# Kernel tuning notes

Measured on AMD Instinct MI355X. Metric: run time of the kernel, lower is better.

Reference implementation:

```python
import jax, jax.numpy as jnp
import numpy as np

B, N, D, S, H = 32, 4096, 256, 16, 512
ITERS = 3
EPS = 1e-8
LN_EPS = 1e-5  # torch LayerNorm default


def _ln(x, w, b):
    m = jnp.mean(x, axis=-1, keepdims=True)
    v = jnp.mean(jnp.square(x - m), axis=-1, keepdims=True)
    return (x - m) / jnp.sqrt(v + LN_EPS) * w + b


def setup_inputs() -> dict:
    key = jax.random.key(0)
    ks = jax.random.split(key, 20)
    s = 1.0 / np.sqrt(D)
    return {
        "inputs": jax.random.normal(ks[0], (B, N, D), jnp.float32),
        "token_weight": jax.random.uniform(ks[1], (B, N), jnp.float32),
        "noise": jax.random.normal(ks[2], (B, S, D), jnp.float32),
        "ln_in_w": jnp.ones((D,), jnp.float32), "ln_in_b": jnp.zeros((D,), jnp.float32),
        "ln_s_w": jnp.ones((D,), jnp.float32), "ln_s_b": jnp.zeros((D,), jnp.float32),
        "ln_m_w": jnp.ones((D,), jnp.float32), "ln_m_b": jnp.zeros((D,), jnp.float32),
        "Wk": jax.random.normal(ks[3], (D, D), jnp.float32) * s,
        "Wv": jax.random.normal(ks[4], (D, D), jnp.float32) * s,
        "Wq": jax.random.normal(ks[5], (D, D), jnp.float32) * s,
        "gru_wih": jax.random.normal(ks[6], (3 * D, D), jnp.float32) * s,
        "gru_whh": jax.random.normal(ks[7], (3 * D, D), jnp.float32) * s,
        "gru_bih": jax.random.normal(ks[8], (3 * D,), jnp.float32) * s,
        "gru_bhh": jax.random.normal(ks[9], (3 * D,), jnp.float32) * s,
        "mlp_w1": jax.random.normal(ks[10], (H, D), jnp.float32) * s,
        "mlp_b1": jnp.zeros((H,), jnp.float32),
        "mlp_w2": jax.random.normal(ks[11], (D, H), jnp.float32) * (1.0 / np.sqrt(H)),
        "mlp_b2": jnp.zeros((D,), jnp.float32),
        "slots_mu": jax.random.normal(ks[12], (1, 1, D), jnp.float32) * 0.02,
        "slots_logsigma": jax.random.normal(ks[13], (1, 1, D), jnp.float32) * 0.02,
    }


def _gru(x, h, wih, whh, bih, bhh):
    # torch GRUCell: gates ordered r, z, n
    gi = x @ wih.T + bih  # [BS, 3D]
    gh = h @ whh.T + bhh
    ir, iz, inn = jnp.split(gi, 3, axis=-1)
    hr, hz, hn = jnp.split(gh, 3, axis=-1)
    r = jax.nn.sigmoid(ir + hr)
    z = jax.nn.sigmoid(iz + hz)
    n = jnp.tanh(inn + r * hn)
    return (1.0 - z) * n + z * h


def reference(inputs, token_weight, noise, ln_in_w, ln_in_b, ln_s_w, ln_s_b,
              ln_m_w, ln_m_b, Wk, Wv, Wq, gru_wih, gru_whh, gru_bih, gru_bhh,
              mlp_w1, mlp_b1, mlp_w2, mlp_b2, slots_mu, slots_logsigma):
    tw = jnp.clip(token_weight, 0.0, None)  # [B,N]
    x = _ln(inputs, ln_in_w, ln_in_b)
    k = x @ Wk.T  # [B,N,D]
    v = x @ Wv.T
    sigma = jnp.clip(jnp.exp(slots_logsigma), 1e-6, None)
    slots = slots_mu + sigma * noise  # [B,S,D]
    scale = D ** (-0.5)
    attn = None
    for _ in range(ITERS):
        slots_prev = slots
        q = _ln(slots, ln_s_w, ln_s_b) @ Wq.T  # [B,S,D]
        logits = jnp.einsum('bnd,bmd->bnm', k, q) * scale  # [B,N,S]
        attn = jax.nn.softmax(logits, axis=-1)  # softmax over slots
        attn = attn * tw[:, :, None]
        attn = attn / (jnp.sum(attn, axis=1, keepdims=True) + EPS)  # normalize over tokens
        updates = jnp.einsum('bnm,bnd->bmd', attn, v)  # [B,S,D]
        slots = _gru(updates.reshape(B * S, D), slots_prev.reshape(B * S, D),
                     gru_wih, gru_whh, gru_bih, gru_bhh).reshape(B, S, D)
        h = jax.nn.gelu(_ln(slots, ln_m_w, ln_m_b) @ mlp_w1.T + mlp_b1, approximate=False)
        slots = slots + h @ mlp_w2.T + mlp_b2
    return slots, attn
```

## Files before the change

### kernel.cpp

```cpp
#include <hip/hip_runtime.h>
#include <hip/hip_bf16.h>
#include <math.h>


#define EPS_ 1e-8f
#define LNEPS_ 1e-5f
#define XSW(r) ((((r)&7)<<3) ^ ((((r)>>3)&3)<<4))

typedef __attribute__((ext_vector_type(8))) short bf16x8;
typedef __attribute__((ext_vector_type(4))) float f32x4;
typedef __attribute__((ext_vector_type(4))) short s16x4;

static __device__ __forceinline__ short f2bf(float f) {
  __hip_bfloat16 h = __float2bfloat16(f);
  union { __hip_bfloat16 h; short s; } u; u.h = h; return u.s;
}
static __device__ __forceinline__ float4 ld4(const float* p){ return *(const float4*)p; }

__global__ __launch_bounds__(256) void k_prep(
    const float* __restrict__ Wq, const float* __restrict__ Wk,
    const float* __restrict__ wih, const float* __restrict__ Wv,
    const float* __restrict__ whh, const float* __restrict__ w1, const float* __restrict__ w2,
    short* __restrict__ MTb, short* __restrict__ Mb, short* __restrict__ whhb,
    short* __restrict__ w1b, short* __restrict__ w2b) {
  int blk = blockIdx.x, t = threadIdx.x;
  if (blk < 64) {
    int e0 = blk*4;
    float a0=0,a1=0,a2=0,a3=0;
    for (int d=0; d<256; d++) {
      float qv = Wq[d*256 + t];
      a0 += qv*Wk[d*256+e0];   a1 += qv*Wk[d*256+e0+1];
      a2 += qv*Wk[d*256+e0+2]; a3 += qv*Wk[d*256+e0+3];
    }
    MTb[(e0  )*256+t]=f2bf(a0); MTb[(e0+1)*256+t]=f2bf(a1);
    MTb[(e0+2)*256+t]=f2bf(a2); MTb[(e0+3)*256+t]=f2bf(a3);
  } else if (blk < 256) {
    int n0 = (blk-64)*4;
    float a0=0,a1=0,a2=0,a3=0;
    for (int d=0; d<256; d++) {
      float vv = Wv[d*256 + t];
      a0 += wih[(n0  )*256+d]*vv; a1 += wih[(n0+1)*256+d]*vv;
      a2 += wih[(n0+2)*256+d]*vv; a3 += wih[(n0+3)*256+d]*vv;
    }
    Mb[(size_t)(n0  )*256+t]=f2bf(a0); Mb[(size_t)(n0+1)*256+t]=f2bf(a1);
    Mb[(size_t)(n0+2)*256+t]=f2bf(a2); Mb[(size_t)(n0+3)*256+t]=f2bf(a3);
  } else {
    int c = (blk-256)*256 + t;
    const float* src; short* dst;
    if (c < 49152) { src=whh; dst=whhb; }
    else if ((c-=49152) < 32768) { src=w1; dst=w1b; }
    else { c-=32768; src=w2; dst=w2b; }
    float4 v = ld4(src + (size_t)c*4);
    short4 o; o.x=f2bf(v.x); o.y=f2bf(v.y); o.z=f2bf(v.z); o.w=f2bf(v.w);
    *(short4*)(dst + (size_t)c*4) = o;
  }
}

template<int LNIN, int WATTN>
__global__ __launch_bounds__(256) void k3(
    const float* __restrict__ inputs, const float* __restrict__ lnw, const float* __restrict__ lnb,
    short* __restrict__ xbf, const short* __restrict__ qk, const float* __restrict__ twg,
    float* __restrict__ ux_part, float* __restrict__ colsum_part, float* __restrict__ attn_un) {
  __shared__ __align__(16) short Xs[64*256];
  __shared__ __align__(16) short Pt[16*72];
  __shared__ float tws[64];
  __shared__ float cs[16];
  __shared__ float lnwb[512];
  const int t = threadIdx.x;
  const int b = blockIdx.x >> 6;
  const size_t rowbase = (size_t)b*4096 + (blockIdx.x & 63)*64;
  const int lane = t & 63, w = t >> 6, l15 = lane & 15, lg = lane >> 4;
  if (t<64) tws[t] = fmaxf(twg[rowbase + t], 0.f);
  if (t<16) cs[t]=0.f;
  bf16x8 qkf[8];
  {
    const short* qrow = qk + ((size_t)(b*16+l15))*256 + lg*8;
    #pragma unroll
    for (int kk=0;kk<8;kk++) qkf[kk] = *(const bf16x8*)(qrow + kk*32);
  }
  if (LNIN) {
    if (t < 64)       *(float4*)&lnwb[t*4]           = ld4(lnw + t*4);
    else if (t < 128) *(float4*)&lnwb[256+(t-64)*4]  = ld4(lnb + (t-64)*4);
    __syncthreads();
    const float* ing = inputs + rowbase*256;
    const int r = t>>2, c = t&3;
    float4 vv[16];
    #pragma unroll
    for (int k=0;k<16;k++) vv[k] = ld4(ing + r*256 + (c+4*k)*4);
    float s=0.f, sq=0.f;
    #pragma unroll
    for (int k=0;k<16;k++){
      s  += vv[k].x+vv[k].y+vv[k].z+vv[k].w;
      sq += vv[k].x*vv[k].x+vv[k].y*vv[k].y+vv[k].z*vv[k].z+vv[k].w*vv[k].w;
    }
    s += __shfl_xor(s,1);  s += __shfl_xor(s,2);
    sq += __shfl_xor(sq,1); sq += __shfl_xor(sq,2);
    float mean = s*(1.f/256.f);
    float rstd = rsqrtf(sq*(1.f/256.f) - mean*mean + LNEPS_);
    short* xw = xbf + rowbase*256;
    const int sw = XSW(r);
    #pragma unroll
    for (int k=0;k<16;k++){
      int d0 = (c+4*k)*4;
      float4 wv = *(float4*)&lnwb[d0];
      float4 bv = *(float4*)&lnwb[256+d0];
      s16x4 pk;
      pk[0]=f2bf((vv[k].x-mean)*rstd*wv.x+bv.x);
      pk[1]=f2bf((vv[k].y-mean)*rstd*wv.y+bv.y);
      pk[2]=f2bf((vv[k].z-mean)*rstd*wv.z+bv.z);
      pk[3]=f2bf((vv[k].w-mean)*rstd*wv.w+bv.w);
      *(s16x4*)&Xs[r*256 + (d0 ^ sw)] = pk;
      *(s16x4*)&xw[r*256 + d0] = pk;
    }
  } else {
    const int srow = t>>5, sck = t&31;
    uint4 pf[8];
    const short* xg = xbf + rowbase*256;
    #pragma unroll
    for (int r8=0;r8<8;r8++)
      pf[r8] = *(const uint4*)&xg[(size_t)(r8*8+srow)*256 + sck*8];
    #pragma unroll
    for (int r8=0;r8<8;r8++){
      int row = r8*8+srow;
      *(uint4*)&Xs[row*256 + ((sck*8) ^ XSW(row))] = pf[r8];
    }
  }
  __syncthreads();
  f32x4 acc = {0.f,0.f,0.f,0.f};
  {
    const int ra = w*16+l15, sa = XSW(ra);
    #pragma unroll
    for (int kk=0;kk<8;kk++){
      bf16x8 af = *(const bf16x8*)&Xs[ra*256 + ((kk*32+lg*8) ^ sa)];
      acc = __builtin_amdgcn_mfma_f32_16x16x32_bf16(af, qkf[kk], acc, 0,0,0);
    }
  }
  float a4[4];
  #pragma unroll
  for (int q=0;q<4;q++){
    float v = acc[q]*0.0625f;
    float m = v;
    #pragma unroll
    for (int d=1; d<16; d<<=1) m = fmaxf(m, __shfl_xor(m, d, 16));
    float e = __expf(v-m);
    float se = e;
    #pragma unroll
    for (int d=1; d<16; d<<=1) se += __shfl_xor(se, d, 16);
    int row = w*16 + lg*4 + q;
    float a = (e/se)*tws[row];
    a4[q] = a;
    if (WATTN)
      attn_un[(rowbase + row)*16 + l15] = a;
  }
  float psum = a4[0]+a4[1]+a4[2]+a4[3];
  psum += __shfl_xor(psum, 16);
  psum += __shfl_xor(psum, 32);
  if (lane<16) atomicAdd(&cs[l15], psum);
  s16x4 pk; pk[0]=f2bf(a4[0]); pk[1]=f2bf(a4[1]); pk[2]=f2bf(a4[2]); pk[3]=f2bf(a4[3]);
  *(s16x4*)&Pt[l15*72 + w*16 + lg*4] = pk;
  __syncthreads();
  f32x4 uacc[4] = {};
  #pragma unroll
  for (int kk=0;kk<2;kk++){
    bf16x8 a2 = *(const bf16x8*)&Pt[l15*72 + kk*32 + lg*8];
    #pragma unroll
    for (int tt=0;tt<4;tt++){
      int col = w*64 + tt*16 + l15;
      bf16x8 b2;
      #pragma unroll
      for (int j=0;j<8;j++){
        int r2 = kk*32 + lg*8 + j;
        b2[j] = Xs[r2*256 + (col ^ XSW(r2))];
      }
      uacc[tt] = __builtin_amdgcn_mfma_f32_16x16x32_bf16(a2, b2, uacc[tt], 0,0,0);
    }
  }
  if (t<16) colsum_part[blockIdx.x*16 + t] = cs[t];
  #pragma unroll
  for (int tt=0;tt<4;tt++){
    #pragma unroll
    for (int q=0;q<4;q++)
      ux_part[(size_t)blockIdx.x*4096 + (lg*4+q)*256 + w*64 + tt*16 + l15] = uacc[tt][q];
  }
}

__global__ __launch_bounds__(256) void k_reduce(const float* __restrict__ uxp,
    const float* __restrict__ csp, short* __restrict__ uxr, float* __restrict__ csr) {
  int r = blockIdx.x;
  int b = r>>4, s = r&15;
  int t = threadIdx.x;
  float cs = 0.f;
  #pragma unroll 8
  for (int k=0;k<64;k++) cs += csp[((b<<6)+k)*16 + s];
  float u = 0.f;
  #pragma unroll 8
  for (int k=0;k<64;k++) u += uxp[(size_t)((b<<6)+k)*4096 + s*256 + t];
  uxr[(size_t)r*256+t] = f2bf(u/(cs+EPS_));
  if (t==0) csr[r] = cs;
}

__global__ __launch_bounds__(256) void k_gigh(
    const short* __restrict__ uxr, const short* __restrict__ slotsb,
    const short* __restrict__ Mb, const short* __restrict__ whhb,
    const float* __restrict__ bih, const float* __restrict__ bhh,
    float* __restrict__ gig) {
  __shared__ short As[64*40];
  __shared__ short Ws[64*40];
  const int t=threadIdx.x, bn=blockIdx.x, bm=blockIdx.y;
  const short* A; const short* W; const float* bias; int wo;
  if (bn<12) { A=uxr;    W=Mb   + (size_t)bn*64*256;      bias=bih; wo=bn*64; }
  else       { A=slotsb; W=whhb + (size_t)(bn-12)*64*256; bias=bhh; wo=(bn-12)*64; }
  const int w=t>>6, lane=t&63, l15=lane&15, lg=lane>>4;
  f32x4 acc[4]={};
  for (int k0=0;k0<256;k0+=32){
    __syncthreads();
    *(uint4*)&As[(t>>2)*40+(t&3)*8] = *(const uint4*)&A[(size_t)(bm*64+(t>>2))*256 + k0 + (t&3)*8];
    *(uint4*)&Ws[(t>>2)*40+(t&3)*8] = *(const uint4*)&W[(size_t)(t>>2)*256 + k0 + (t&3)*8];
    __syncthreads();
    bf16x8 af = *(const bf16x8*)&As[(w*16+l15)*40+lg*8];
    #pragma unroll
    for (int ct=0;ct<4;ct++){
      bf16x8 bfr = *(const bf16x8*)&Ws[(ct*16+l15)*40+lg*8];
      acc[ct]=__builtin_amdgcn_mfma_f32_16x16x32_bf16(af,bfr,acc[ct],0,0,0);
    }
  }
  #pragma unroll
  for (int ct=0;ct<4;ct++){
    float bv = bias[wo + ct*16 + l15];
    #pragma unroll
    for (int q=0;q<4;q++){
      int row = bm*64 + w*16 + lg*4 + q;
      gig[(size_t)row*1536 + bn*64 + ct*16 + l15] = acc[ct][q] + bv;
    }
  }
}

__global__ __launch_bounds__(256) void k_mlp1(
    const short* __restrict__ lnmb, const short* __restrict__ w1b,
    const float* __restrict__ b1, short* __restrict__ hb) {
  __shared__ short As[64*40];
  __shared__ short Ws[64*40];
  const int t=threadIdx.x, bn=blockIdx.x, bm=blockIdx.y;
  const int w=t>>6, lane=t&63, l15=lane&15, lg=lane>>4;
  f32x4 acc[4]={};
  for (int k0=0;k0<256;k0+=32){
    __syncthreads();
    *(uint4*)&As[(t>>2)*40+(t&3)*8] = *(const uint4*)&lnmb[(size_t)(bm*64+(t>>2))*256 + k0 + (t&3)*8];
    *(uint4*)&Ws[(t>>2)*40+(t&3)*8] = *(const uint4*)&w1b[(size_t)(bn*64+(t>>2))*256 + k0 + (t&3)*8];
    __syncthreads();
    bf16x8 af = *(const bf16x8*)&As[(w*16+l15)*40+lg*8];
    #pragma unroll
    for (int ct=0;ct<4;ct++){
      bf16x8 bfr = *(const bf16x8*)&Ws[(ct*16+l15)*40+lg*8];
      acc[ct]=__builtin_amdgcn_mfma_f32_16x16x32_bf16(af,bfr,acc[ct],0,0,0);
    }
  }
  #pragma unroll
  for (int ct=0;ct<4;ct++){
    float bv = b1[bn*64 + ct*16 + l15];
    #pragma unroll
    for (int q=0;q<4;q++){
      int row = bm*64 + w*16 + lg*4 + q;
      float v = acc[ct][q] + bv;
      v = 0.5f*v*(1.f+erff(v*0.70710678118654752f));
      hb[(size_t)row*512 + bn*64 + ct*16 + l15] = f2bf(v);
    }
  }
}

__global__ __launch_bounds__(256) void k_gates(const float* __restrict__ gig,
    const float* __restrict__ lw, const float* __restrict__ lb,
    float* __restrict__ slots, short* __restrict__ lnmb) {
  int row  = blockIdx.x*4 + (threadIdx.x>>6);
  int lane = threadIdx.x & 63;
  const float* gi = gig + (size_t)row*1536 + lane*4;
  float4 ir = ld4(gi), iz = ld4(gi+256), inn = ld4(gi+512);
  float4 hr = ld4(gi+768), hz = ld4(gi+1024), hn = ld4(gi+1280);
  float* sp = slots + (size_t)row*256 + lane*4;
  float4 h = ld4(sp);
  float hp[4];
  {
    float r0 = 1.f/(1.f+__expf(-(ir.x+hr.x))); float z0 = 1.f/(1.f+__expf(-(iz.x+hz.x)));
    hp[0] = (1.f-z0)*tanhf(inn.x + r0*hn.x) + z0*h.x;
    float r1 = 1.f/(1.f+__expf(-(ir.y+hr.y))); float z1 = 1.f/(1.f+__expf(-(iz.y+hz.y)));
    hp[1] = (1.f-z1)*tanhf(inn.y + r1*hn.y) + z1*h.y;
    float r2 = 1.f/(1.f+__expf(-(ir.z+hr.z))); float z2 = 1.f/(1.f+__expf(-(iz.z+hz.z)));
    hp[2] = (1.f-z2)*tanhf(inn.z + r2*hn.z) + z2*h.z;
    float r3 = 1.f/(1.f+__expf(-(ir.w+hr.w))); float z3 = 1.f/(1.f+__expf(-(iz.w+hz.w)));
    hp[3] = (1.f-z3)*tanhf(inn.w + r3*hn.w) + z3*h.w;
  }
  float s = hp[0]+hp[1]+hp[2]+hp[3];
  float sq = hp[0]*hp[0]+hp[1]*hp[1]+hp[2]*hp[2]+hp[3]*hp[3];
  #pragma unroll
  for (int d=1; d<64; d<<=1) { s += __shfl_xor(s,d); sq += __shfl_xor(sq,d); }
  float mean = s*(1.f/256.f);
  float rstd = rsqrtf(sq*(1.f/256.f) - mean*mean + LNEPS_);
  float4 wv = ld4(lw+lane*4), bv = ld4(lb+lane*4);
  *(float4*)sp = make_float4(hp[0],hp[1],hp[2],hp[3]);
  short4 o;
  o.x = f2bf((hp[0]-mean)*rstd*wv.x+bv.x);
  o.y = f2bf((hp[1]-mean)*rstd*wv.y+bv.y);
  o.z = f2bf((hp[2]-mean)*rstd*wv.z+bv.z);
  o.w = f2bf((hp[3]-mean)*rstd*wv.w+bv.w);
  *(short4*)(lnmb + (size_t)row*256 + lane*4) = o;
}

template<int MODE>
__global__ __launch_bounds__(256) void k_slotend(
    const short* __restrict__ hb, const short* __restrict__ w2b, const float* __restrict__ b2,
    const float* __restrict__ mu, const float* __restrict__ ls, const float* __restrict__ noise,
    const float* __restrict__ res, float* __restrict__ sout, short* __restrict__ slotsb,
    const float* __restrict__ lnsw, const float* __restrict__ lnsb,
    const short* __restrict__ MTb, short* __restrict__ qk) {
  __shared__ short As[64*40];
  __shared__ short Ws[256*40];
  __shared__ short lnS[64*264];
  const int t=threadIdx.x, bm=blockIdx.x;
  const int w=t>>6, lane=t&63, l15=lane&15, lg=lane>>4;
  float v[16][4];
  if (MODE==1) {
    #pragma unroll
    for (int ct=0;ct<16;ct++){
      int col = ct*16+l15;
      float m = mu[col], sg = fmaxf(__expf(ls[col]),1e-6f);
      #pragma unroll
      for (int q=0;q<4;q++){
        int row = bm*64 + w*16 + lg*4 + q;
        v[ct][q] = m + sg*noise[(size_t)row*256+col];
      }
    }
  } else {
    f32x4 acc[16]={};
    for (int k0=0;k0<512;k0+=32){
      __syncthreads();
      *(uint4*)&As[(t>>2)*40+(t&3)*8] = *(const uint4*)&hb[(size_t)(bm*64+(t>>2))*512 + k0 + (t&3)*8];
      #pragma unroll
      for (int i=0;i<4;i++){ int idx=t+i*256;
        *(uint4*)&Ws[(idx>>2)*40+(idx&3)*8] = *(const uint4*)&w2b[(size_t)(idx>>2)*512 + k0 + (idx&3)*8]; }
      __syncthreads();
      bf16x8 af = *(const bf16x8*)&As[(w*16+l15)*40+lg*8];
      #pragma unroll
      for (int ct=0;ct<16;ct++){
        bf16x8 bfr = *(const bf16x8*)&Ws[(ct*16+l15)*40+lg*8];
        acc[ct]=__builtin_amdgcn_mfma_f32_16x16x32_bf16(af,bfr,acc[ct],0,0,0);
      }
    }
    #pragma unroll
    for (int ct=0;ct<16;ct++){
      int col = ct*16+l15;
      float bv = b2[col];
      #pragma unroll
      for (int q=0;q<4;q++){
        int row = bm*64 + w*16 + lg*4 + q;
        v[ct][q] = acc[ct][q] + bv + res[(size_t)row*256+col];
      }
    }
  }
  float s[4]={0,0,0,0}, sq[4]={0,0,0,0};
  #pragma unroll
  for (int ct=0;ct<16;ct++)
    #pragma unroll
    for (int q=0;q<4;q++){ s[q]+=v[ct][q]; sq[q]+=v[ct][q]*v[ct][q]; }
  #pragma unroll
  for (int q=0;q<4;q++){
    #pragma unroll
    for (int d=1; d<16; d<<=1){ s[q]+=__shfl_xor(s[q],d,16); sq[q]+=__shfl_xor(sq[q],d,16); }
  }
  #pragma unroll
  for (int ct=0;ct<16;ct++){
    int col = ct*16+l15;
    float lw = (MODE!=2) ? lnsw[col] : 0.f;
    float lb = (MODE!=2) ? lnsb[col] : 0.f;
    #pragma unroll
    for (int q=0;q<4;q++){
      int row = bm*64 + w*16 + lg*4 + q;
      sout[(size_t)row*256+col] = v[ct][q];
      if (MODE!=2){
        float mean = s[q]*(1.f/256.f);
        float rstd = rsqrtf(sq[q]*(1.f/256.f)-mean*mean+LNEPS_);
        slotsb[(size_t)row*256+col] = f2bf(v[ct][q]);
        lnS[(w*16+lg*4+q)*264 + col] = f2bf((v[ct][q]-mean)*rstd*lw+lb);
      }
    }
  }
  if (MODE!=2){
    f32x4 qa[16]={};
    for (int k0=0;k0<256;k0+=32){
      __syncthreads();
      #pragma unroll
      for (int i=0;i<4;i++){ int idx=t+i*256;
        *(uint4*)&Ws[(idx>>2)*40+(idx&3)*8] = *(const uint4*)&MTb[(size_t)(idx>>2)*256 + k0 + (idx&3)*8]; }
      __syncthreads();
      bf16x8 af = *(const bf16x8*)&lnS[(w*16+l15)*264 + k0 + lg*8];
      #pragma unroll
      for (int ct=0;ct<16;ct++){
        bf16x8 bfr = *(const bf16x8*)&Ws[(ct*16+l15)*40+lg*8];
        qa[ct]=__builtin_amdgcn_mfma_f32_16x16x32_bf16(af,bfr,qa[ct],0,0,0);
      }
    }
    #pragma unroll
    for (int ct=0;ct<16;ct++)
      #pragma unroll
      for (int q=0;q<4;q++)
        qk[(size_t)(bm*64+w*16+lg*4+q)*256 + ct*16+l15] = f2bf(qa[ct][q]);
  }
}

__global__ __launch_bounds__(256) void k_attn_norm(float* __restrict__ au,
    const float* __restrict__ cs) {
  size_t i = ((size_t)blockIdx.x*256 + threadIdx.x)*4;
  float4 v = ld4(au + i);
  int s = (int)(i & 15);
  size_t b = i >> 16;
  const float* c = cs + b*16 + s;
  float4 o;
  o.x = v.x/(c[0]+EPS_); o.y = v.y/(c[1]+EPS_);
  o.z = v.z/(c[2]+EPS_); o.w = v.w/(c[3]+EPS_);
  *(float4*)(au + i) = o;
}

extern "C" void kernel_launch(void* const* d_in, const int* in_sizes, int n_in,
                              void* d_out, int out_size, void* d_ws, size_t ws_size,
                              hipStream_t stream) {
  const float* inputs   = (const float*)d_in[0];
  const float* token_w  = (const float*)d_in[1];
  const float* noise    = (const float*)d_in[2];
  const float* ln_in_w  = (const float*)d_in[3];
  const float* ln_in_b  = (const float*)d_in[4];
  const float* ln_s_w   = (const float*)d_in[5];
  const float* ln_s_b   = (const float*)d_in[6];
  const float* ln_m_w   = (const float*)d_in[7];
  const float* ln_m_b   = (const float*)d_in[8];
  const float* Wk       = (const float*)d_in[9];
  const float* Wv       = (const float*)d_in[10];
  const float* Wq       = (const float*)d_in[11];
  const float* gru_wih  = (const float*)d_in[12];
  const float* gru_whh  = (const float*)d_in[13];
  const float* gru_bih  = (const float*)d_in[14];
  const float* gru_bhh  = (const float*)d_in[15];
  const float* mlp_w1   = (const float*)d_in[16];
  const float* mlp_b1   = (const float*)d_in[17];
  const float* mlp_w2   = (const float*)d_in[18];
  const float* mlp_b2   = (const float*)d_in[19];
  const float* slots_mu = (const float*)d_in[20];
  const float* slots_ls = (const float*)d_in[21];

  float* out_slots = (float*)d_out;
  float* out_attn  = out_slots + 131072;

  char* wsb = (char*)d_ws;
  size_t off = 0;
  short* xbf     = (short*)(wsb + off); off += 67108864;
  float* ux_part = (float*)(wsb + off); off += 33554432;
  float* cs_part = (float*)(wsb + off); off += 131072;
  float* cs_red  = (float*)(wsb + off); off += 2048;
  short* qk      = (short*)(wsb + off); off += 262144;
  short* uxr     = (short*)(wsb + off); off += 262144;
  short* MTb     = (short*)(wsb + off); off += 131072;
  short* Mb      = (short*)(wsb + off); off += 393216;
  float* gig     = (float*)(wsb + off); off += 3145728;
  float* slots   = (float*)(wsb + off); off += 524288;
  short* slotsb  = (short*)(wsb + off); off += 262144;
  short* lnmb    = (short*)(wsb + off); off += 262144;
  short* hb      = (short*)(wsb + off); off += 524288;
  short* whhb    = (short*)(wsb + off); off += 393216;
  short* w1b     = (short*)(wsb + off); off += 262144;
  short* w2b     = (short*)(wsb + off); off += 262144;

  k_prep<<<704,256,0,stream>>>(Wq, Wk, gru_wih, Wv, gru_whh, mlp_w1, mlp_w2,
                               MTb, Mb, whhb, w1b, w2b);
  k_slotend<1><<<8,256,0,stream>>>(nullptr, nullptr, nullptr, slots_mu, slots_ls, noise,
                                   nullptr, slots, slotsb, ln_s_w, ln_s_b, MTb, qk);
  for (int it=0; it<3; ++it) {
    if (it==0)
      k3<1,0><<<2048,256,0,stream>>>(inputs, ln_in_w, ln_in_b, xbf, qk, token_w,
                                     ux_part, cs_part, out_attn);
    else if (it==1)
      k3<0,0><<<2048,256,0,stream>>>(inputs, ln_in_w, ln_in_b, xbf, qk, token_w,
                                     ux_part, cs_part, out_attn);
    else
      k3<0,1><<<2048,256,0,stream>>>(inputs, ln_in_w, ln_in_b, xbf, qk, token_w,
                                     ux_part, cs_part, out_attn);
    k_reduce<<<512,256,0,stream>>>(ux_part, cs_part, uxr, cs_red);
    k_gigh<<<dim3(24,8),256,0,stream>>>(uxr, slotsb, Mb, whhb, gru_bih, gru_bhh, gig);
    k_gates<<<128,256,0,stream>>>(gig, ln_m_w, ln_m_b, slots, lnmb);
    k_mlp1<<<dim3(8,8),256,0,stream>>>(lnmb, w1b, mlp_b1, hb);
    if (it<2)
      k_slotend<0><<<8,256,0,stream>>>(hb, w2b, mlp_b2, nullptr, nullptr, nullptr,
                                       slots, slots, slotsb, ln_s_w, ln_s_b, MTb, qk);
    else
      k_slotend<2><<<8,256,0,stream>>>(hb, w2b, mlp_b2, nullptr, nullptr, nullptr,
                                       slots, out_slots, slotsb, ln_s_w, ln_s_b, MTb, qk);
  }
  k_attn_norm<<<2048,256,0,stream>>>(out_attn, cs_red);
}
```

Measured before the change: 262.0 us.

## Halve k3 row tile to 32 and store partial updates as bf16

The k3 attention kernel now processes 32 tokens per block instead of 64 and launches twice as many blocks with a launch-bounds occupancy hint. LDS use drops, but only two of four waves do the logits/softmax MFMA. Per-block partial update sums are staged through shared memory and written as bf16 with vector stores, and k_reduce sums 128 bf16 partials per batch instead of 64 fp32 ones. The aim is higher occupancy and less partial-sum traffic, at the cost of more partials to reduce, idle waves in the first phase, and lower precision in the accumulated partials.

```diff
diff --git a/kernel.cpp b/kernel.cpp
--- a/kernel.cpp
+++ b/kernel.cpp
@@ -14,6 +14,9 @@
 static __device__ __forceinline__ short f2bf(float f) {
   __hip_bfloat16 h = __float2bfloat16(f);
   union { __hip_bfloat16 h; short s; } u; u.h = h; return u.s;
+}
+static __device__ __forceinline__ float bf2f(short s) {
+  union { float f; unsigned u; } x; x.u = ((unsigned)(unsigned short)s) << 16; return x.f;
 }
 static __device__ __forceinline__ float4 ld4(const float* p){ return *(const float4*)p; }
 
@@ -57,23 +60,23 @@
 }
 
 template<int LNIN, int WATTN>
-__global__ __launch_bounds__(256) void k3(
+__global__ __launch_bounds__(256, 6) void k3(
     const float* __restrict__ inputs, const float* __restrict__ lnw, const float* __restrict__ lnb,
     short* __restrict__ xbf, const short* __restrict__ qk, const float* __restrict__ twg,
-    float* __restrict__ ux_part, float* __restrict__ colsum_part, float* __restrict__ attn_un) {
-  __shared__ __align__(16) short Xs[64*256];
-  __shared__ __align__(16) short Pt[16*72];
-  __shared__ float tws[64];
+    short* __restrict__ ux_part, float* __restrict__ colsum_part, float* __restrict__ attn_un) {
+  __shared__ __align__(16) short Xs[32*256];
+  __shared__ __align__(16) short Pt[16*40];
+  __shared__ float tws[32];
   __shared__ float cs[16];
   __shared__ float lnwb[512];
   const int t = threadIdx.x;
-  const int b = blockIdx.x >> 6;
-  const size_t rowbase = (size_t)b*4096 + (blockIdx.x & 63)*64;
+  const int b = blockIdx.x >> 7;
+  const size_t rowbase = (size_t)b*4096 + (blockIdx.x & 127)*32;
   const int lane = t & 63, w = t >> 6, l15 = lane & 15, lg = lane >> 4;
-  if (t<64) tws[t] = fmaxf(twg[rowbase + t], 0.f);
+  if (t<32) tws[t] = fmaxf(twg[rowbase + t], 0.f);
   if (t<16) cs[t]=0.f;
   bf16x8 qkf[8];
-  {
+  if (w<2) {
     const short* qrow = qk + ((size_t)(b*16+l15))*256 + lg*8;
     #pragma unroll
     for (int kk=0;kk<8;kk++) qkf[kk] = *(const bf16x8*)(qrow + kk*32);
@@ -83,25 +86,25 @@
     else if (t < 128) *(float4*)&lnwb[256+(t-64)*4]  = ld4(lnb + (t-64)*4);
     __syncthreads();
     const float* ing = inputs + rowbase*256;
-    const int r = t>>2, c = t&3;
-    float4 vv[16];
-    #pragma unroll
-    for (int k=0;k<16;k++) vv[k] = ld4(ing + r*256 + (c+4*k)*4);
+    const int r = t>>3, c = t&7;
+    float4 vv[8];
+    #pragma unroll
+    for (int k=0;k<8;k++) vv[k] = ld4(ing + r*256 + (c+8*k)*4);
     float s=0.f, sq=0.f;
     #pragma unroll
-    for (int k=0;k<16;k++){
+    for (int k=0;k<8;k++){
       s  += vv[k].x+vv[k].y+vv[k].z+vv[k].w;
       sq += vv[k].x*vv[k].x+vv[k].y*vv[k].y+vv[k].z*vv[k].z+vv[k].w*vv[k].w;
     }
-    s += __shfl_xor(s,1);  s += __shfl_xor(s,2);
-    sq += __shfl_xor(sq,1); sq += __shfl_xor(sq,2);
+    s += __shfl_xor(s,1);  s += __shfl_xor(s,2);  s += __shfl_xor(s,4);
+    sq += __shfl_xor(sq,1); sq += __shfl_xor(sq,2); sq += __shfl_xor(sq,4);
     float mean = s*(1.f/256.f);
     float rstd = rsqrtf(sq*(1.f/256.f) - mean*mean + LNEPS_);
     short* xw = xbf + rowbase*256;
     const int sw = XSW(r);
     #pragma unroll
-    for (int k=0;k<16;k++){
-      int d0 = (c+4*k)*4;
+    for (int k=0;k<8;k++){
+      int d0 = (c+8*k)*4;
       float4 wv = *(float4*)&lnwb[d0];
       float4 bv = *(float4*)&lnwb[256+d0];
       s16x4 pk;
@@ -113,88 +116,95 @@
       *(s16x4*)&xw[r*256 + d0] = pk;
     }
   } else {
-    const int srow = t>>5, sck = t&31;
-    uint4 pf[8];
+    uint4 pf[4];
     const short* xg = xbf + rowbase*256;
     #pragma unroll
-    for (int r8=0;r8<8;r8++)
-      pf[r8] = *(const uint4*)&xg[(size_t)(r8*8+srow)*256 + sck*8];
-    #pragma unroll
-    for (int r8=0;r8<8;r8++){
-      int row = r8*8+srow;
-      *(uint4*)&Xs[row*256 + ((sck*8) ^ XSW(row))] = pf[r8];
+    for (int i=0;i<4;i++){
+      int idx = t + i*256;
+      pf[i] = *(const uint4*)&xg[(size_t)(idx>>5)*256 + (idx&31)*8];
+    }
+    #pragma unroll
+    for (int i=0;i<4;i++){
+      int idx = t + i*256, row = idx>>5;
+      *(uint4*)&Xs[row*256 + (((idx&31)*8) ^ XSW(row))] = pf[i];
     }
   }
   __syncthreads();
-  f32x4 acc = {0.f,0.f,0.f,0.f};
-  {
+  if (w<2) {
+    f32x4 acc = {0.f,0.f,0.f,0.f};
     const int ra = w*16+l15, sa = XSW(ra);
     #pragma unroll
     for (int kk=0;kk<8;kk++){
       bf16x8 af = *(const bf16x8*)&Xs[ra*256 + ((kk*32+lg*8) ^ sa)];
       acc = __builtin_amdgcn_mfma_f32_16x16x32_bf16(af, qkf[kk], acc, 0,0,0);
     }
-  }
-  float a4[4];
-  #pragma unroll
-  for (int q=0;q<4;q++){
-    float v = acc[q]*0.0625f;
-    float m = v;
-    #pragma unroll
-    for (int d=1; d<16; d<<=1) m = fmaxf(m, __shfl_xor(m, d, 16));
-    float e = __expf(v-m);
-    float se = e;
-    #pragma unroll
-    for (int d=1; d<16; d<<=1) se += __shfl_xor(se, d, 16);
-    int row = w*16 + lg*4 + q;
-    float a = (e/se)*tws[row];
-    a4[q] = a;
-    if (WATTN)
-      attn_un[(rowbase + row)*16 + l15] = a;
-  }
-  float psum = a4[0]+a4[1]+a4[2]+a4[3];
-  psum += __shfl_xor(psum, 16);
-  psum += __shfl_xor(psum, 32);
-  if (lane<16) atomicAdd(&cs[l15], psum);
-  s16x4 pk; pk[0]=f2bf(a4[0]); pk[1]=f2bf(a4[1]); pk[2]=f2bf(a4[2]); pk[3]=f2bf(a4[3]);
-  *(s16x4*)&Pt[l15*72 + w*16 + lg*4] = pk;
+    float a4[4];
+    #pragma unroll
+    for (int q=0;q<4;q++){
+      float v = acc[q]*0.0625f;
+      float m = v;
+      #pragma unroll
+      for (int d=1; d<16; d<<=1) m = fmaxf(m, __shfl_xor(m, d, 16));
+      float e = __expf(v-m);
+      float se = e;
+      #pragma unroll
+      for (int d=1; d<16; d<<=1) se += __shfl_xor(se, d, 16);
+      int row = w*16 + lg*4 + q;
+      float a = (e/se)*tws[row];
+      a4[q] = a;
+      if (WATTN)
+        attn_un[(rowbase + row)*16 + l15] = a;
+    }
+    float psum = a4[0]+a4[1]+a4[2]+a4[3];
+    psum += __shfl_xor(psum, 16);
+    psum += __shfl_xor(psum, 32);
+    if (lane<16) atomicAdd(&cs[l15], psum);
+    s16x4 pk; pk[0]=f2bf(a4[0]); pk[1]=f2bf(a4[1]); pk[2]=f2bf(a4[2]); pk[3]=f2bf(a4[3]);
+    *(s16x4*)&Pt[l15*40 + w*16 + lg*4] = pk;
+  }
   __syncthreads();
   f32x4 uacc[4] = {};
-  #pragma unroll
-  for (int kk=0;kk<2;kk++){
-    bf16x8 a2 = *(const bf16x8*)&Pt[l15*72 + kk*32 + lg*8];
+  {
+    bf16x8 a2 = *(const bf16x8*)&Pt[l15*40 + lg*8];
     #pragma unroll
     for (int tt=0;tt<4;tt++){
       int col = w*64 + tt*16 + l15;
       bf16x8 b2;
       #pragma unroll
       for (int j=0;j<8;j++){
-        int r2 = kk*32 + lg*8 + j;
+        int r2 = lg*8 + j;
         b2[j] = Xs[r2*256 + (col ^ XSW(r2))];
       }
       uacc[tt] = __builtin_amdgcn_mfma_f32_16x16x32_bf16(a2, b2, uacc[tt], 0,0,0);
     }
   }
   if (t<16) colsum_part[blockIdx.x*16 + t] = cs[t];
-  #pragma unroll
-  for (int tt=0;tt<4;tt++){
+  __syncthreads();
+  #pragma unroll
+  for (int tt=0;tt<4;tt++)
     #pragma unroll
     for (int q=0;q<4;q++)
-      ux_part[(size_t)blockIdx.x*4096 + (lg*4+q)*256 + w*64 + tt*16 + l15] = uacc[tt][q];
-  }
-}
-
-__global__ __launch_bounds__(256) void k_reduce(const float* __restrict__ uxp,
+      Xs[(lg*4+q)*256 + w*64 + tt*16 + l15] = f2bf(uacc[tt][q]);
+  __syncthreads();
+  short* up = ux_part + (size_t)blockIdx.x*4096;
+  #pragma unroll
+  for (int i=0;i<2;i++){
+    int idx = t + i*256;
+    *(uint4*)&up[idx*8] = *(const uint4*)&Xs[idx*8];
+  }
+}
+
+__global__ __launch_bounds__(256) void k_reduce(const short* __restrict__ uxp,
     const float* __restrict__ csp, short* __restrict__ uxr, float* __restrict__ csr) {
   int r = blockIdx.x;
   int b = r>>4, s = r&15;
   int t = threadIdx.x;
   float cs = 0.f;
   #pragma unroll 8
-  for (int k=0;k<64;k++) cs += csp[((b<<6)+k)*16 + s];
+  for (int k=0;k<128;k++) cs += csp[((b<<7)+k)*16 + s];
   float u = 0.f;
   #pragma unroll 8
-  for (int k=0;k<64;k++) u += uxp[(size_t)((b<<6)+k)*4096 + s*256 + t];
+  for (int k=0;k<128;k++) u += bf2f(uxp[(size_t)((b<<7)+k)*4096 + s*256 + t]);
   uxr[(size_t)r*256+t] = f2bf(u/(cs+EPS_));
   if (t==0) csr[r] = cs;
 }
@@ -451,8 +461,8 @@
   char* wsb = (char*)d_ws;
   size_t off = 0;
   short* xbf     = (short*)(wsb + off); off += 67108864;
-  float* ux_part = (float*)(wsb + off); off += 33554432;
-  float* cs_part = (float*)(wsb + off); off += 131072;
+  short* ux_part = (short*)(wsb + off); off += 33554432;
+  float* cs_part = (float*)(wsb + off); off += 262144;
   float* cs_red  = (float*)(wsb + off); off += 2048;
   short* qk      = (short*)(wsb + off); off += 262144;
   short* uxr     = (short*)(wsb + off); off += 262144;
@@ -473,13 +483,13 @@
                                    nullptr, slots, slotsb, ln_s_w, ln_s_b, MTb, qk);
   for (int it=0; it<3; ++it) {
     if (it==0)
-      k3<1,0><<<2048,256,0,stream>>>(inputs, ln_in_w, ln_in_b, xbf, qk, token_w,
+      k3<1,0><<<4096,256,0,stream>>>(inputs, ln_in_w, ln_in_b, xbf, qk, token_w,
                                      ux_part, cs_part, out_attn);
     else if (it==1)
-      k3<0,0><<<2048,256,0,stream>>>(inputs, ln_in_w, ln_in_b, xbf, qk, token_w,
+      k3<0,0><<<4096,256,0,stream>>>(inputs, ln_in_w, ln_in_b, xbf, qk, token_w,
                                      ux_part, cs_part, out_attn);
     else
-      k3<0,1><<<2048,256,0,stream>>>(inputs, ln_in_w, ln_in_b, xbf, qk, token_w,
+      k3<0,1><<<4096,256,0,stream>>>(inputs, ln_in_w, ln_in_b, xbf, qk, token_w,
                                      ux_part, cs_part, out_attn);
     k_reduce<<<512,256,0,stream>>>(ux_part, cs_part, uxr, cs_red);
     k_gigh<<<dim3(24,8),256,0,stream>>>(uxr, slotsb, Mb, whhb, gru_bih, gru_bhh, gig);
```

New measurement: 330.2 us. +26.1%, slower.
